# Kernel optimization log

Hardware: AMD Instinct MI355X
Metric: run time of the kernel (lower is better)

Reference implementation:

```python
import jax, jax.numpy as jnp
import numpy as np

N = 4096      # nodes
HID = 512     # hidden_size
HEADS = 8
DH = HID // HEADS
EPS = 1e-5    # BatchNorm eps


def setup_inputs() -> dict:
    key = jax.random.key(0)
    ks = jax.random.split(key, 16)
    h = jax.random.normal(ks[0], (N, HID), jnp.float32)
    # sparse adjacency (~degree 32) with self-loops so every row has a neighbor
    A = (jax.random.uniform(ks[1], (N, N)) < 0.008).astype(jnp.float32)
    A = jnp.maximum(A, jnp.eye(N, dtype=jnp.float32))
    w = lambda k, shp: jax.random.normal(k, shp, jnp.float32) * 0.02
    return {
        "A": A, "h": h,
        "Wq": w(ks[2], (HID, HID)), "bq": jnp.zeros((HID,), jnp.float32),
        "Wk": w(ks[3], (HID, HID)), "bk": jnp.zeros((HID,), jnp.float32),
        "Wv": w(ks[4], (HID, HID)), "bv": jnp.zeros((HID,), jnp.float32),
        "Wo": w(ks[5], (HID, HID)), "bo": jnp.zeros((HID,), jnp.float32),
        "bn1_g": jnp.ones((HID,), jnp.float32), "bn1_b": jnp.zeros((HID,), jnp.float32),
        "bn2_g": jnp.ones((HID,), jnp.float32), "bn2_b": jnp.zeros((HID,), jnp.float32),
        "W1": w(ks[6], (HID, 2 * HID)), "b1": jnp.zeros((2 * HID,), jnp.float32),
        "W2": w(ks[7], (2 * HID, HID)), "b2": jnp.zeros((HID,), jnp.float32),
    }


def _batchnorm(x, g, b):
    # BatchNorm1d training mode: stats over the node (batch) axis
    m = jnp.mean(x, axis=0)
    v = jnp.var(x, axis=0)
    return g * (x - m) * jax.lax.rsqrt(v + EPS) + b


def _layer(A, h, Wq, bq, Wk, bk, Wv, bv, Wo, bo,
           bn1_g, bn1_b, bn2_g, bn2_b, W1, b1, W2, b2):
    n = h.shape[0]
    q = (h @ Wq + bq).reshape(n, HEADS, DH)
    k = (h @ Wk + bk).reshape(n, HEADS, DH)
    v = (h @ Wv + bv).reshape(n, HEADS, DH)
    # scores [heads, n, m], masked by adjacency
    scores = jnp.einsum('nhd,mhd->hnm', q, k) / np.float32(np.sqrt(DH))
    scores = jnp.where(A[None, :, :] > 0, scores, jnp.float32(-1e9))
    attn = jax.nn.softmax(scores, axis=-1)
    o = jnp.einsum('hnm,mhd->nhd', attn, v).reshape(n, HID)
    h1 = o @ Wo + bo
    h = _batchnorm(h + h1, bn1_g, bn1_b)
    h2 = jax.nn.relu(h @ W1 + b1) @ W2 + b2
    return _batchnorm(h + h2, bn2_g, bn2_b)


def reference(A, h, Wq, bq, Wk, bk, Wv, bv, Wo, bo,
              bn1_g, bn1_b, bn2_g, bn2_b, W1, b1, W2, b2):
    return _layer(A, h, Wq, bq, Wk, bk, Wv, bv, Wo, bo,
                  bn1_g, bn1_b, bn2_g, bn2_b, W1, b1, W2, b2)
```

## Files before the change

### kernel.cpp

```cpp
#include <hip/hip_runtime.h>

#define N_NODES 4096
#define HID 512
#define HEADS 8
#define DH 64
#define EPS 1e-5f
#define MAXD 128

typedef __attribute__((ext_vector_type(8))) short bf16x8;
typedef __attribute__((ext_vector_type(4))) float f32x4;

__device__ __forceinline__ unsigned short f2bf(float f) {
    unsigned int u = __float_as_uint(f);
    unsigned int r = (u + 0x7FFFu + ((u >> 16) & 1u)) >> 16;
    return (unsigned short)r;
}
__device__ __forceinline__ float blo(unsigned int u) {
    return __uint_as_float(u << 16);
}
__device__ __forceinline__ float bhi(unsigned int u) {
    return __uint_as_float(u & 0xffff0000u);
}

__device__ __forceinline__ void gld_lds16(const void* g, void* l) {
    __builtin_amdgcn_global_load_lds(
        (const __attribute__((address_space(1))) unsigned int*)g,
        (__attribute__((address_space(3))) unsigned int*)l, 16, 0, 0);
}

template<int TM, int EPI>
__global__ __launch_bounds__(256) void gemm_bf16(
    const unsigned short* __restrict__ Xb, const unsigned short* __restrict__ Wt,
    const float* __restrict__ bias, const float* __restrict__ res,
    const unsigned short* __restrict__ resb,
    float* __restrict__ outf, unsigned short* __restrict__ outb,
    float* __restrict__ sum, float* __restrict__ sumsq,
    int K, int Nc)
{
    constexpr int WM = TM / 64;
    __shared__ __align__(16) unsigned short As[TM * 64];
    __shared__ __align__(16) unsigned short Bs[64 * 64];

    const int tid = threadIdx.x;
    const int lane = tid & 63;
    const int wv = tid >> 6;
    const int m0 = blockIdx.y * TM, n0 = blockIdx.x * 64;
    const int lc = lane & 15, lq = lane >> 4;
    const int rowbase = wv * (WM * 16);

    const int srow = tid >> 3;
    const int schunk = (tid & 7) ^ (srow & 7);
    unsigned short* ldsA = As + tid * 8;
    unsigned short* ldsB = Bs + tid * 8;
    const int rs0 = lq ^ (lc & 7);
    const int rs1 = (4 + lq) ^ (lc & 7);

    f32x4 acc[WM][4] = {};

    for (int k0 = 0; k0 < K; k0 += 64) {
        const unsigned short* gA = Xb + (size_t)(m0 + srow) * K + k0 + schunk * 8;
        const unsigned short* gB = Wt + (size_t)(n0 + srow) * K + k0 + schunk * 8;
        #pragma unroll
        for (int p = 0; p < TM / 32; ++p)
            gld_lds16(gA + (size_t)(p * 32) * K, ldsA + p * 2048);
        #pragma unroll
        for (int p = 0; p < 2; ++p)
            gld_lds16(gB + (size_t)(p * 32) * K, ldsB + p * 2048);
        __syncthreads();

        #pragma unroll
        for (int hh = 0; hh < 2; ++hh) {
            const int rs = hh ? rs1 : rs0;
            bf16x8 af[WM], bfr[4];
            #pragma unroll
            for (int i = 0; i < WM; ++i)
                af[i] = *(const bf16x8*)&As[(rowbase + i * 16 + lc) * 64 + rs * 8];
            #pragma unroll
            for (int j = 0; j < 4; ++j)
                bfr[j] = *(const bf16x8*)&Bs[(j * 16 + lc) * 64 + rs * 8];
            #pragma unroll
            for (int i = 0; i < WM; ++i)
                #pragma unroll
                for (int j = 0; j < 4; ++j)
                    acc[i][j] = __builtin_amdgcn_mfma_f32_16x16x32_bf16(af[i], bfr[j], acc[i][j], 0, 0, 0);
        }
        __syncthreads();
    }

    float cs[4] = {}, css[4] = {};
    #pragma unroll
    for (int i = 0; i < WM; ++i) {
        #pragma unroll
        for (int j = 0; j < 4; ++j) {
            const int gr0 = m0 + rowbase + i * 16 + lq * 4;
            const int gc = n0 + j * 16 + lc;
            const float bi = bias[gc];
            #pragma unroll
            for (int r = 0; r < 4; ++r) {
                float val = acc[i][j][r] + bi;
                size_t off = (size_t)(gr0 + r) * Nc + gc;
                if (EPI == 0)      outb[off] = f2bf(val);
                else if (EPI == 1) outb[off] = f2bf(fmaxf(val, 0.f));
                else {
                    if (EPI == 2) val += res[off];
                    else          val += blo((unsigned int)resb[off]);
                    outf[off] = val;
                    cs[j] += val; css[j] += val * val;
                }
            }
        }
    }
    if (EPI >= 2) {
        #pragma unroll
        for (int j = 0; j < 4; ++j) {
            float s = cs[j], ss = css[j];
            s += __shfl_xor(s, 16); s += __shfl_xor(s, 32);
            ss += __shfl_xor(ss, 16); ss += __shfl_xor(ss, 32);
            if (lq == 0) {
                const int gc = n0 + j * 16 + lc;
                atomicAdd(&sum[gc], s);
                atomicAdd(&sumsq[gc], ss);
            }
        }
    }
}

__global__ __launch_bounds__(256) void prep_all(
    const float* __restrict__ Wq, const float* __restrict__ Wk,
    const float* __restrict__ Wv, const float* __restrict__ Wo,
    const float* __restrict__ W1, const float* __restrict__ W2,
    const float* __restrict__ h,
    const float* __restrict__ bq, const float* __restrict__ bk,
    const float* __restrict__ bv,
    unsigned short* __restrict__ wqkvT, unsigned short* __restrict__ woT,
    unsigned short* __restrict__ w1T, unsigned short* __restrict__ w2T,
    unsigned int* __restrict__ hb, float* __restrict__ bqkv,
    float* __restrict__ st)
{
    const int z = blockIdx.z;
    if (z < 6) {
        const float* in; unsigned short* out; int R, C;
        switch (z) {
            case 0: in = Wq; out = wqkvT;          R = 512;  C = 512;  break;
            case 1: in = Wk; out = wqkvT + 262144; R = 512;  C = 512;  break;
            case 2: in = Wv; out = wqkvT + 524288; R = 512;  C = 512;  break;
            case 3: in = Wo; out = woT;            R = 512;  C = 512;  break;
            case 4: in = W1; out = w1T;            R = 512;  C = 1024; break;
            default: in = W2; out = w2T;           R = 1024; C = 512;  break;
        }
        const int bc = blockIdx.x * 32, br = blockIdx.y * 32;
        if (bc >= C || br >= R) return;
        __shared__ float tile[32][33];
        const int tx = threadIdx.x & 31, ty = threadIdx.x >> 5;
        #pragma unroll
        for (int r = ty; r < 32; r += 8)
            tile[r][tx] = in[(size_t)(br + r) * C + bc + tx];
        __syncthreads();
        #pragma unroll
        for (int r = ty; r < 32; r += 8)
            out[(size_t)(bc + r) * R + br + tx] = f2bf(tile[tx][r]);
    } else if (z == 6) {
        const int blk = blockIdx.y * 32 + blockIdx.x;
        const int i = blk * 512 + threadIdx.x * 2;
        const float4* in4 = (const float4*)h;
        #pragma unroll
        for (int u = 0; u < 2; ++u) {
            float4 f = in4[i + u];
            hb[(i + u) * 2]     = (unsigned int)f2bf(f.x) | ((unsigned int)f2bf(f.y) << 16);
            hb[(i + u) * 2 + 1] = (unsigned int)f2bf(f.z) | ((unsigned int)f2bf(f.w) << 16);
        }
    } else {
        const int blk = blockIdx.y * 32 + blockIdx.x;
        const int i = blk * 256 + threadIdx.x;
        if (i < 1536) bqkv[i] = i < 512 ? bq[i] : (i < 1024 ? bk[i - 512] : bv[i - 1024]);
        if (i < 2048) st[i] = 0.0f;
    }
}

__global__ __launch_bounds__(256) void sparse_attn5(
    const float* __restrict__ A, const unsigned short* __restrict__ qkv,
    unsigned short* __restrict__ o)
{
    const int n = blockIdx.x;
    const int tid = threadIdx.x;
    const int wv = tid >> 6, lane = tid & 63;

    __shared__ int s_idx[MAXD];
    __shared__ float s_p[8][MAXD];
    __shared__ int s_cnt[4];

    const float4* r4 = (const float4*)(A + (size_t)n * N_NODES);
    float4 av[4];
    #pragma unroll
    for (int t = 0; t < 4; ++t)
        av[t] = r4[wv * 256 + t * 64 + lane];

    const unsigned long long lt = (1ull << lane) - 1ull;
    int cnt = 0;
    #pragma unroll
    for (int t = 0; t < 4; ++t) {
        #pragma unroll
        for (int b = 0; b < 4; ++b) {
            float vb = (b == 0) ? av[t].x : (b == 1) ? av[t].y : (b == 2) ? av[t].z : av[t].w;
            cnt += __popcll(__ballot(vb > 0.0f));
        }
    }
    if (lane == 0) s_cnt[wv] = cnt;
    __syncthreads();
    int base = 0, total = 0;
    #pragma unroll
    for (int w = 0; w < 4; ++w) {
        if (w < wv) base += s_cnt[w];
        total += s_cnt[w];
    }
    const int d = total < MAXD ? total : MAXD;
    #pragma unroll
    for (int t = 0; t < 4; ++t) {
        #pragma unroll
        for (int b = 0; b < 4; ++b) {
            float vb = (b == 0) ? av[t].x : (b == 1) ? av[t].y : (b == 2) ? av[t].z : av[t].w;
            unsigned long long m = __ballot(vb > 0.0f);
            if (vb > 0.0f) {
                int p = base + __popcll(m & lt);
                if (p < MAXD) s_idx[p] = wv * 1024 + t * 256 + lane * 4 + b;
            }
            base += __popcll(m);
        }
    }
    __syncthreads();

    const int jl = lane >> 3;
    const int dgs = lane & 7;
    const int jl2 = lane >> 4;
    const int dga = lane & 15;
    const int h0 = wv, h1 = wv + 4;

    const unsigned short* qp = qkv + (size_t)n * 1536 + dgs * 8;
    uint4 qa = *(const uint4*)(qp + h0 * 64);
    uint4 qb = *(const uint4*)(qp + h1 * 64);
    const float a0 = blo(qa.x), a1 = bhi(qa.x), a2 = blo(qa.y), a3 = bhi(qa.y);
    const float a4 = blo(qa.z), a5 = bhi(qa.z), a6 = blo(qa.w), a7 = bhi(qa.w);
    const float b0 = blo(qb.x), b1 = bhi(qb.x), b2 = blo(qb.y), b3 = bhi(qb.y);
    const float b4 = blo(qb.z), b5 = bhi(qb.z), b6 = blo(qb.w), b7 = bhi(qb.w);

    uint4 ka = {0, 0, 0, 0}, kb = {0, 0, 0, 0};
    if (jl < d) {
        const unsigned short* p = qkv + (size_t)s_idx[jl] * 1536 + 512 + dgs * 8;
        ka = *(const uint4*)(p + h0 * 64);
        kb = *(const uint4*)(p + h1 * 64);
    }
    for (int j0 = 0; j0 < d; j0 += 8) {
        const uint4 ca = ka, cb = kb;
        const int jn = j0 + 8 + jl;
        if (jn < d) {
            const unsigned short* p = qkv + (size_t)s_idx[jn] * 1536 + 512 + dgs * 8;
            ka = *(const uint4*)(p + h0 * 64);
            kb = *(const uint4*)(p + h1 * 64);
        }
        const int jc = j0 + jl;
        float s0 = 0.f, s1 = 0.f;
        if (jc < d) {
            s0 = a0 * blo(ca.x) + a1 * bhi(ca.x) + a2 * blo(ca.y) + a3 * bhi(ca.y)
               + a4 * blo(ca.z) + a5 * bhi(ca.z) + a6 * blo(ca.w) + a7 * bhi(ca.w);
            s1 = b0 * blo(cb.x) + b1 * bhi(cb.x) + b2 * blo(cb.y) + b3 * bhi(cb.y)
               + b4 * blo(cb.z) + b5 * bhi(cb.z) + b6 * blo(cb.w) + b7 * bhi(cb.w);
        }
        s0 += __shfl_xor(s0, 1); s1 += __shfl_xor(s1, 1);
        s0 += __shfl_xor(s0, 2); s1 += __shfl_xor(s1, 2);
        s0 += __shfl_xor(s0, 4); s1 += __shfl_xor(s1, 4);
        if (dgs == 0 && jc < d) {
            s_p[h0][jc] = s0 * 0.125f;
            s_p[h1][jc] = s1 * 0.125f;
        }
    }

    float inv0, inv1;
    #pragma unroll
    for (int hh = 0; hh < 2; ++hh) {
        float* sp = s_p[hh ? h1 : h0];
        float mx = -1e30f;
        for (int j = lane; j < d; j += 64) mx = fmaxf(mx, sp[j]);
        #pragma unroll
        for (int off = 32; off; off >>= 1) mx = fmaxf(mx, __shfl_xor(mx, off));
        float sum = 0.f;
        for (int j = lane; j < d; j += 64) {
            float e = __expf(sp[j] - mx);
            sp[j] = e;
            sum += e;
        }
        #pragma unroll
        for (int off = 32; off; off >>= 1) sum += __shfl_xor(sum, off);
        if (hh) inv1 = 1.0f / sum; else inv0 = 1.0f / sum;
    }

    float x0 = 0.f, x1 = 0.f, x2 = 0.f, x3 = 0.f;
    float y0 = 0.f, y1 = 0.f, y2 = 0.f, y3 = 0.f;
    uint2 va = {0, 0}, vb = {0, 0};
    if (jl2 < d) {
        const unsigned short* p = qkv + (size_t)s_idx[jl2] * 1536 + 1024 + dga * 4;
        va = *(const uint2*)(p + h0 * 64);
        vb = *(const uint2*)(p + h1 * 64);
    }
    for (int j0 = 0; j0 < d; j0 += 4) {
        const uint2 ca = va, cb = vb;
        const int jn = j0 + 4 + jl2;
        if (jn < d) {
            const unsigned short* p = qkv + (size_t)s_idx[jn] * 1536 + 1024 + dga * 4;
            va = *(const uint2*)(p + h0 * 64);
            vb = *(const uint2*)(p + h1 * 64);
        }
        const int jc = j0 + jl2;
        if (jc < d) {
            const float p0 = s_p[h0][jc], p1 = s_p[h1][jc];
            x0 += p0 * blo(ca.x); x1 += p0 * bhi(ca.x);
            x2 += p0 * blo(ca.y); x3 += p0 * bhi(ca.y);
            y0 += p1 * blo(cb.x); y1 += p1 * bhi(cb.x);
            y2 += p1 * blo(cb.y); y3 += p1 * bhi(cb.y);
        }
    }
    x0 += __shfl_xor(x0, 16); x0 += __shfl_xor(x0, 32);
    x1 += __shfl_xor(x1, 16); x1 += __shfl_xor(x1, 32);
    x2 += __shfl_xor(x2, 16); x2 += __shfl_xor(x2, 32);
    x3 += __shfl_xor(x3, 16); x3 += __shfl_xor(x3, 32);
    y0 += __shfl_xor(y0, 16); y0 += __shfl_xor(y0, 32);
    y1 += __shfl_xor(y1, 16); y1 += __shfl_xor(y1, 32);
    y2 += __shfl_xor(y2, 16); y2 += __shfl_xor(y2, 32);
    y3 += __shfl_xor(y3, 16); y3 += __shfl_xor(y3, 32);
    if (jl2 == 0) {
        uint2 w0, w1;
        w0.x = (unsigned int)f2bf(x0 * inv0) | ((unsigned int)f2bf(x1 * inv0) << 16);
        w0.y = (unsigned int)f2bf(x2 * inv0) | ((unsigned int)f2bf(x3 * inv0) << 16);
        w1.x = (unsigned int)f2bf(y0 * inv1) | ((unsigned int)f2bf(y1 * inv1) << 16);
        w1.y = (unsigned int)f2bf(y2 * inv1) | ((unsigned int)f2bf(y3 * inv1) << 16);
        *(uint2*)(o + (size_t)n * 512 + h0 * 64 + dga * 4) = w0;
        *(uint2*)(o + (size_t)n * 512 + h1 * 64 + dga * 4) = w1;
    }
}

__global__ __launch_bounds__(256) void bn_apply4(
    const float4* __restrict__ x, const float* __restrict__ sum,
    const float* __restrict__ sumsq, const float* __restrict__ g,
    const float* __restrict__ b, float4* __restrict__ yf,
    uint2* __restrict__ yb)
{
    const int i = blockIdx.x * 256 + threadIdx.x;
    const int c4 = i & 127;
    const float4 s4 = ((const float4*)sum)[c4];
    const float4 q4 = ((const float4*)sumsq)[c4];
    const float4 g4 = ((const float4*)g)[c4];
    const float4 b4 = ((const float4*)b)[c4];
    const float4 xv = x[i];
    const float kN = 1.0f / N_NODES;
    float4 r;
    { float m = s4.x * kN; r.x = g4.x * (xv.x - m) * rsqrtf(q4.x * kN - m * m + EPS) + b4.x; }
    { float m = s4.y * kN; r.y = g4.y * (xv.y - m) * rsqrtf(q4.y * kN - m * m + EPS) + b4.y; }
    { float m = s4.z * kN; r.z = g4.z * (xv.z - m) * rsqrtf(q4.z * kN - m * m + EPS) + b4.z; }
    { float m = s4.w * kN; r.w = g4.w * (xv.w - m) * rsqrtf(q4.w * kN - m * m + EPS) + b4.w; }
    if (yf) yf[i] = r;
    if (yb) {
        uint2 p;
        p.x = (unsigned int)f2bf(r.x) | ((unsigned int)f2bf(r.y) << 16);
        p.y = (unsigned int)f2bf(r.z) | ((unsigned int)f2bf(r.w) << 16);
        yb[i] = p;
    }
}


extern "C" void kernel_launch(void* const* d_in, const int* in_sizes, int n_in,
                              void* d_out, int out_size, void* d_ws, size_t ws_size,
                              hipStream_t stream)
{
    const float* A   = (const float*)d_in[0];
    const float* h   = (const float*)d_in[1];
    const float* Wq  = (const float*)d_in[2];
    const float* bq  = (const float*)d_in[3];
    const float* Wk  = (const float*)d_in[4];
    const float* bk  = (const float*)d_in[5];
    const float* Wv  = (const float*)d_in[6];
    const float* bv  = (const float*)d_in[7];
    const float* Wo  = (const float*)d_in[8];
    const float* bo  = (const float*)d_in[9];
    const float* g1  = (const float*)d_in[10];
    const float* b1g = (const float*)d_in[11];
    const float* g2  = (const float*)d_in[12];
    const float* b2g = (const float*)d_in[13];
    const float* W1  = (const float*)d_in[14];
    const float* b1  = (const float*)d_in[15];
    const float* W2  = (const float*)d_in[16];
    const float* b2  = (const float*)d_in[17];
    float* out = (float*)d_out;

    float* ws = (float*)d_ws;
    unsigned short* hb    = (unsigned short*)(ws);
    unsigned short* qkvb  = (unsigned short*)(ws + 1048576);
    unsigned short* o_bf  = (unsigned short*)(ws + 4194304);
    unsigned short* wqkvT = (unsigned short*)(ws + 5242880);
    unsigned short* woT   = (unsigned short*)(ws + 5636096);
    unsigned short* w1T   = (unsigned short*)(ws + 5767168);
    unsigned short* w2T   = (unsigned short*)(ws + 6029312);
    unsigned short* t_b   = (unsigned short*)(ws + 6291456);
    float* x1   = ws + 8388608;
    float* x2   = ws + 10485760;
    unsigned short* xb1_b = (unsigned short*)(ws + 12582912);
    float* bqkv = ws + 13631488;
    float* st   = ws + 13633024;

    prep_all<<<dim3(32, 32, 8), dim3(256), 0, stream>>>(
        Wq, Wk, Wv, Wo, W1, W2, h, bq, bk, bv,
        wqkvT, woT, w1T, w2T, (unsigned int*)hb, bqkv, st);

    gemm_bf16<128, 0><<<dim3(24, 32), dim3(256), 0, stream>>>(
        hb, wqkvT, bqkv, nullptr, nullptr, nullptr, qkvb, nullptr, nullptr, 512, 1536);

    sparse_attn5<<<dim3(N_NODES), dim3(256), 0, stream>>>(A, qkvb, o_bf);

    gemm_bf16<64, 2><<<dim3(8, 64), dim3(256), 0, stream>>>(
        o_bf, woT, bo, h, nullptr, x1, nullptr, st, st + 512, 512, 512);

    bn_apply4<<<dim3(2048), dim3(256), 0, stream>>>(
        (const float4*)x1, st, st + 512, g1, b1g, nullptr, (uint2*)xb1_b);

    gemm_bf16<128, 1><<<dim3(16, 32), dim3(256), 0, stream>>>(
        xb1_b, w1T, b1, nullptr, nullptr, nullptr, t_b, nullptr, nullptr, 512, 1024);

    gemm_bf16<64, 3><<<dim3(8, 64), dim3(256), 0, stream>>>(
        t_b, w2T, b2, nullptr, xb1_b, x2, nullptr, st + 1024, st + 1536, 1024, 512);

    bn_apply4<<<dim3(2048), dim3(256), 0, stream>>>(
        (const float4*)x2, st + 1024, st + 1536, g2, b2g, (float4*)out, nullptr);

    (void)in_sizes; (void)n_in; (void)out_size; (void)ws_size;
}
```

Before: 232.9 us.

## Replace LDS-staged GEMM with single-wave direct-global-load MFMA kernel

The bf16 GEMM drops its shared-memory staging (global_load_lds plus swizzled LDS reads and two block barriers per k-step). Each 64-thread block now computes a small TMx64 tile, loading MFMA fragments straight from global memory into registers. The grids are resized to many more, smaller blocks. This removes barrier and LDS overhead and raises block count, but gives up data reuse across waves, so each operand is fetched from global or L2 more times, and the loads are strided 16-byte per-lane accesses.

```diff
diff --git a/kernel.cpp b/kernel.cpp
--- a/kernel.cpp
+++ b/kernel.cpp
@@ -22,14 +22,8 @@
     return __uint_as_float(u & 0xffff0000u);
 }
 
-__device__ __forceinline__ void gld_lds16(const void* g, void* l) {
-    __builtin_amdgcn_global_load_lds(
-        (const __attribute__((address_space(1))) unsigned int*)g,
-        (__attribute__((address_space(3))) unsigned int*)l, 16, 0, 0);
-}
-
 template<int TM, int EPI>
-__global__ __launch_bounds__(256) void gemm_bf16(
+__global__ __launch_bounds__(64) void gemm_w1(
     const unsigned short* __restrict__ Xb, const unsigned short* __restrict__ Wt,
     const float* __restrict__ bias, const float* __restrict__ res,
     const unsigned short* __restrict__ resb,
@@ -37,54 +31,36 @@
     float* __restrict__ sum, float* __restrict__ sumsq,
     int K, int Nc)
 {
-    constexpr int WM = TM / 64;
-    __shared__ __align__(16) unsigned short As[TM * 64];
-    __shared__ __align__(16) unsigned short Bs[64 * 64];
-
-    const int tid = threadIdx.x;
-    const int lane = tid & 63;
-    const int wv = tid >> 6;
+    constexpr int WM = TM / 16;
+    const int lane = threadIdx.x;
     const int m0 = blockIdx.y * TM, n0 = blockIdx.x * 64;
     const int lc = lane & 15, lq = lane >> 4;
-    const int rowbase = wv * (WM * 16);
-
-    const int srow = tid >> 3;
-    const int schunk = (tid & 7) ^ (srow & 7);
-    unsigned short* ldsA = As + tid * 8;
-    unsigned short* ldsB = Bs + tid * 8;
-    const int rs0 = lq ^ (lc & 7);
-    const int rs1 = (4 + lq) ^ (lc & 7);
+
+    const unsigned short* pa = Xb + (size_t)(m0 + lc) * K + lq * 8;
+    const unsigned short* pb = Wt + (size_t)(n0 + lc) * K + lq * 8;
 
     f32x4 acc[WM][4] = {};
 
     for (int k0 = 0; k0 < K; k0 += 64) {
-        const unsigned short* gA = Xb + (size_t)(m0 + srow) * K + k0 + schunk * 8;
-        const unsigned short* gB = Wt + (size_t)(n0 + srow) * K + k0 + schunk * 8;
-        #pragma unroll
-        for (int p = 0; p < TM / 32; ++p)
-            gld_lds16(gA + (size_t)(p * 32) * K, ldsA + p * 2048);
-        #pragma unroll
-        for (int p = 0; p < 2; ++p)
-            gld_lds16(gB + (size_t)(p * 32) * K, ldsB + p * 2048);
-        __syncthreads();
-
-        #pragma unroll
-        for (int hh = 0; hh < 2; ++hh) {
-            const int rs = hh ? rs1 : rs0;
-            bf16x8 af[WM], bfr[4];
+        bf16x8 af[WM][2], bfr[4][2];
+        #pragma unroll
+        for (int i = 0; i < WM; ++i)
             #pragma unroll
-            for (int i = 0; i < WM; ++i)
-                af[i] = *(const bf16x8*)&As[(rowbase + i * 16 + lc) * 64 + rs * 8];
+            for (int h = 0; h < 2; ++h)
+                af[i][h] = *(const bf16x8*)(pa + (size_t)(i * 16) * K + k0 + h * 32);
+        #pragma unroll
+        for (int j = 0; j < 4; ++j)
             #pragma unroll
-            for (int j = 0; j < 4; ++j)
-                bfr[j] = *(const bf16x8*)&Bs[(j * 16 + lc) * 64 + rs * 8];
+            for (int h = 0; h < 2; ++h)
+                bfr[j][h] = *(const bf16x8*)(pb + (size_t)(j * 16) * K + k0 + h * 32);
+        #pragma unroll
+        for (int h = 0; h < 2; ++h)
             #pragma unroll
             for (int i = 0; i < WM; ++i)
                 #pragma unroll
                 for (int j = 0; j < 4; ++j)
-                    acc[i][j] = __builtin_amdgcn_mfma_f32_16x16x32_bf16(af[i], bfr[j], acc[i][j], 0, 0, 0);
-        }
-        __syncthreads();
+                    acc[i][j] = __builtin_amdgcn_mfma_f32_16x16x32_bf16(
+                        af[i][h], bfr[j][h], acc[i][j], 0, 0, 0);
     }
 
     float cs[4] = {}, css[4] = {};
@@ -92,7 +68,7 @@
     for (int i = 0; i < WM; ++i) {
         #pragma unroll
         for (int j = 0; j < 4; ++j) {
-            const int gr0 = m0 + rowbase + i * 16 + lq * 4;
+            const int gr0 = m0 + i * 16 + lq * 4;
             const int gc = n0 + j * 16 + lc;
             const float bi = bias[gc];
             #pragma unroll
@@ -409,21 +385,21 @@
         Wq, Wk, Wv, Wo, W1, W2, h, bq, bk, bv,
         wqkvT, woT, w1T, w2T, (unsigned int*)hb, bqkv, st);
 
-    gemm_bf16<128, 0><<<dim3(24, 32), dim3(256), 0, stream>>>(
+    gemm_w1<64, 0><<<dim3(24, 64), dim3(64), 0, stream>>>(
         hb, wqkvT, bqkv, nullptr, nullptr, nullptr, qkvb, nullptr, nullptr, 512, 1536);
 
     sparse_attn5<<<dim3(N_NODES), dim3(256), 0, stream>>>(A, qkvb, o_bf);
 
-    gemm_bf16<64, 2><<<dim3(8, 64), dim3(256), 0, stream>>>(
+    gemm_w1<32, 2><<<dim3(8, 128), dim3(64), 0, stream>>>(
         o_bf, woT, bo, h, nullptr, x1, nullptr, st, st + 512, 512, 512);
 
     bn_apply4<<<dim3(2048), dim3(256), 0, stream>>>(
         (const float4*)x1, st, st + 512, g1, b1g, nullptr, (uint2*)xb1_b);
 
-    gemm_bf16<128, 1><<<dim3(16, 32), dim3(256), 0, stream>>>(
+    gemm_w1<32, 1><<<dim3(16, 128), dim3(64), 0, stream>>>(
         xb1_b, w1T, b1, nullptr, nullptr, nullptr, t_b, nullptr, nullptr, 512, 1024);
 
-    gemm_bf16<64, 3><<<dim3(8, 64), dim3(256), 0, stream>>>(
+    gemm_w1<32, 3><<<dim3(8, 128), dim3(64), 0, stream>>>(
         t_b, w2T, b2, nullptr, xb1_b, x2, nullptr, st + 1024, st + 1536, 1024, 512);
 
     bn_apply4<<<dim3(2048), dim3(256), 0, stream>>>(
```

After: 271.3 us. +16.5%, slower.

## Fuse first BatchNorm into FFN GEMMs and load A fragments directly from pre-tiled layout

Applied to the files above, without the earlier changes.

The first BatchNorm apply kernel is removed. Its normalization is folded into the W1 GEMM's A-operand load, which reads fp32 x1 and applies a per-channel scale/shift table before converting to bf16, and into the W2 GEMM's residual epilogue. The h and attention-output bf16 buffers are now written in an MFMA-fragment-tiled layout, so the QKV and Wo GEMMs load A straight into registers with double buffering instead of staging through LDS. This drops one kernel launch and a round trip of the intermediate through memory. In exchange, the W1 GEMM reads fp32 A with extra ALU and scattered LDS lookups, and the A loads bypass shared memory reuse.

```diff
diff --git a/kernel.cpp b/kernel.cpp
--- a/kernel.cpp
+++ b/kernel.cpp
@@ -28,71 +28,135 @@
         (__attribute__((address_space(3))) unsigned int*)l, 16, 0, 0);
 }
 
-template<int TM, int EPI>
-__global__ __launch_bounds__(256) void gemm_bf16(
-    const unsigned short* __restrict__ Xb, const unsigned short* __restrict__ Wt,
+
+template<int TM, int EPI, int AMODE, int K>
+__global__ __launch_bounds__(256) void gemm_h(
+    const unsigned short* __restrict__ Xb, const float* __restrict__ Xf,
+    const unsigned short* __restrict__ Wt,
     const float* __restrict__ bias, const float* __restrict__ res,
-    const unsigned short* __restrict__ resb,
     float* __restrict__ outf, unsigned short* __restrict__ outb,
     float* __restrict__ sum, float* __restrict__ sumsq,
-    int K, int Nc)
+    const float* __restrict__ bsum, const float* __restrict__ bsumsq,
+    const float* __restrict__ bg, const float* __restrict__ bb,
+    int Nc)
 {
     constexpr int WM = TM / 64;
-    __shared__ __align__(16) unsigned short As[TM * 64];
+    constexpr int KC = K >> 5;
+    constexpr int NS = K >> 6;
     __shared__ __align__(16) unsigned short Bs[64 * 64];
+    __shared__ float2 lut[(AMODE == 2) ? K : 4];
 
     const int tid = threadIdx.x;
     const int lane = tid & 63;
     const int wv = tid >> 6;
     const int m0 = blockIdx.y * TM, n0 = blockIdx.x * 64;
     const int lc = lane & 15, lq = lane >> 4;
-    const int rowbase = wv * (WM * 16);
+    const int wrow = m0 + wv * (TM / 4);
 
     const int srow = tid >> 3;
     const int schunk = (tid & 7) ^ (srow & 7);
-    unsigned short* ldsA = As + tid * 8;
     unsigned short* ldsB = Bs + tid * 8;
-    const int rs0 = lq ^ (lc & 7);
-    const int rs1 = (4 + lq) ^ (lc & 7);
-
+
+    const unsigned short* paf = Xb + ((size_t)(wrow >> 4) * KC) * 512 + lane * 8;
+    const unsigned short* par = Xb + (size_t)(wrow + lc) * K + lq * 8;
+    const float* parf = Xf + (size_t)(wrow + lc) * K + lq * 8;
+
+    if (AMODE == 2) {
+        #pragma unroll
+        for (int c = tid; c < K; c += 256) {
+            float m = bsum[c] * (1.0f / N_NODES);
+            float v = bsumsq[c] * (1.0f / N_NODES) - m * m;
+            float iv = rsqrtf(v + EPS);
+            float sc = bg[c] * iv;
+            lut[c] = make_float2(sc, bb[c] - sc * m);
+        }
+        __syncthreads();
+    }
+
+    bf16x8 afb[2][WM][2];
     f32x4 acc[WM][4] = {};
 
-    for (int k0 = 0; k0 < K; k0 += 64) {
-        const unsigned short* gA = Xb + (size_t)(m0 + srow) * K + k0 + schunk * 8;
-        const unsigned short* gB = Wt + (size_t)(n0 + srow) * K + k0 + schunk * 8;
-        #pragma unroll
-        for (int p = 0; p < TM / 32; ++p)
-            gld_lds16(gA + (size_t)(p * 32) * K, ldsA + p * 2048);
-        #pragma unroll
-        for (int p = 0; p < 2; ++p)
-            gld_lds16(gB + (size_t)(p * 32) * K, ldsB + p * 2048);
+#define LOAD_A(S, BUF)                                                          \
+    if (AMODE != 2) {                                                           \
+        _Pragma("unroll")                                                       \
+        for (int i = 0; i < WM; ++i)                                            \
+            _Pragma("unroll")                                                   \
+            for (int h = 0; h < 2; ++h)                                         \
+                afb[BUF][i][h] = (AMODE == 1)                                   \
+                    ? *(const bf16x8*)(paf + ((size_t)i * KC + 2 * (S) + h) * 512) \
+                    : *(const bf16x8*)(par + (size_t)(i * 16) * K + (S) * 64 + h * 32); \
+    }
+
+    LOAD_A(0, 0)
+    #pragma unroll
+    for (int s = 0; s < NS; ++s) {
+        const unsigned short* gB = Wt + (size_t)(n0 + srow) * K + s * 64 + schunk * 8;
+        gld_lds16(gB, ldsB);
+        gld_lds16(gB + (size_t)32 * K, ldsB + 2048);
         __syncthreads();
 
-        #pragma unroll
-        for (int hh = 0; hh < 2; ++hh) {
-            const int rs = hh ? rs1 : rs0;
-            bf16x8 af[WM], bfr[4];
+        if (s + 1 < NS) { LOAD_A(s + 1, ((s & 1) ^ 1)) }
+
+        bf16x8 afx[WM][2];
+        if (AMODE == 2) {
             #pragma unroll
             for (int i = 0; i < WM; ++i)
-                af[i] = *(const bf16x8*)&As[(rowbase + i * 16 + lc) * 64 + rs * 8];
+                #pragma unroll
+                for (int h = 0; h < 2; ++h) {
+                    const float* p = parf + (size_t)(i * 16) * K + s * 64 + h * 32;
+                    float4 f0 = *(const float4*)p;
+                    float4 f1 = *(const float4*)(p + 4);
+                    const int kb = s * 64 + h * 32 + lq * 8;
+                    float2 l0 = lut[kb], l1 = lut[kb + 1], l2 = lut[kb + 2], l3 = lut[kb + 3];
+                    float2 l4 = lut[kb + 4], l5 = lut[kb + 5], l6 = lut[kb + 6], l7 = lut[kb + 7];
+                    uint4 uu;
+                    uu.x = (unsigned int)f2bf(f0.x * l0.x + l0.y) | ((unsigned int)f2bf(f0.y * l1.x + l1.y) << 16);
+                    uu.y = (unsigned int)f2bf(f0.z * l2.x + l2.y) | ((unsigned int)f2bf(f0.w * l3.x + l3.y) << 16);
+                    uu.z = (unsigned int)f2bf(f1.x * l4.x + l4.y) | ((unsigned int)f2bf(f1.y * l5.x + l5.y) << 16);
+                    uu.w = (unsigned int)f2bf(f1.z * l6.x + l6.y) | ((unsigned int)f2bf(f1.w * l7.x + l7.y) << 16);
+                    afx[i][h] = *(bf16x8*)&uu;
+                }
+        }
+
+        bf16x8 bfr[4][2];
+        #pragma unroll
+        for (int j = 0; j < 4; ++j)
             #pragma unroll
-            for (int j = 0; j < 4; ++j)
-                bfr[j] = *(const bf16x8*)&Bs[(j * 16 + lc) * 64 + rs * 8];
+            for (int h = 0; h < 2; ++h)
+                bfr[j][h] = *(const bf16x8*)&Bs[(j * 16 + lc) * 64 + ((h * 4 + lq) ^ (lc & 7)) * 8];
+
+        #pragma unroll
+        for (int h = 0; h < 2; ++h)
             #pragma unroll
             for (int i = 0; i < WM; ++i)
                 #pragma unroll
                 for (int j = 0; j < 4; ++j)
-                    acc[i][j] = __builtin_amdgcn_mfma_f32_16x16x32_bf16(af[i], bfr[j], acc[i][j], 0, 0, 0);
-        }
+                    acc[i][j] = __builtin_amdgcn_mfma_f32_16x16x32_bf16(
+                        (AMODE == 2) ? afx[i][h] : afb[s & 1][i][h],
+                        bfr[j][h], acc[i][j], 0, 0, 0);
         __syncthreads();
     }
+#undef LOAD_A
+
+    float scj[4], shj[4];
+    if (EPI == 4) {
+        #pragma unroll
+        for (int j = 0; j < 4; ++j) {
+            const int gc = n0 + j * 16 + lc;
+            float m = bsum[gc] * (1.0f / N_NODES);
+            float v = bsumsq[gc] * (1.0f / N_NODES) - m * m;
+            float iv = rsqrtf(v + EPS);
+            scj[j] = bg[gc] * iv;
+            shj[j] = bb[gc] - scj[j] * m;
+        }
+    }
 
     float cs[4] = {}, css[4] = {};
     #pragma unroll
     for (int i = 0; i < WM; ++i) {
         #pragma unroll
         for (int j = 0; j < 4; ++j) {
-            const int gr0 = m0 + rowbase + i * 16 + lq * 4;
+            const int gr0 = wrow + i * 16 + lq * 4;
             const int gc = n0 + j * 16 + lc;
             const float bi = bias[gc];
             #pragma unroll
@@ -103,7 +167,7 @@
                 else if (EPI == 1) outb[off] = f2bf(fmaxf(val, 0.f));
                 else {
                     if (EPI == 2) val += res[off];
-                    else          val += blo((unsigned int)resb[off]);
+                    else          val += scj[j] * res[off] + shj[j];
                     outf[off] = val;
                     cs[j] += val; css[j] += val * val;
                 }
@@ -163,12 +227,16 @@
         const int blk = blockIdx.y * 32 + blockIdx.x;
         const int i = blk * 512 + threadIdx.x * 2;
         const float4* in4 = (const float4*)h;
-        #pragma unroll
-        for (int u = 0; u < 2; ++u) {
-            float4 f = in4[i + u];
-            hb[(i + u) * 2]     = (unsigned int)f2bf(f.x) | ((unsigned int)f2bf(f.y) << 16);
-            hb[(i + u) * 2 + 1] = (unsigned int)f2bf(f.z) | ((unsigned int)f2bf(f.w) << 16);
-        }
+        float4 f0 = in4[i], f1 = in4[i + 1];
+        uint4 w;
+        w.x = (unsigned int)f2bf(f0.x) | ((unsigned int)f2bf(f0.y) << 16);
+        w.y = (unsigned int)f2bf(f0.z) | ((unsigned int)f2bf(f0.w) << 16);
+        w.z = (unsigned int)f2bf(f1.x) | ((unsigned int)f2bf(f1.y) << 16);
+        w.w = (unsigned int)f2bf(f1.z) | ((unsigned int)f2bf(f1.w) << 16);
+        const int m = i >> 7, k = (i & 127) * 4;
+        const size_t off_u4 = ((size_t)(m >> 4) * 16 + (k >> 5)) * 64
+                            + ((k >> 3) & 3) * 16 + (m & 15);
+        ((uint4*)hb)[off_u4] = w;
     } else {
         const int blk = blockIdx.y * 32 + blockIdx.x;
         const int i = blk * 256 + threadIdx.x;
@@ -177,7 +245,7 @@
     }
 }
 
-__global__ __launch_bounds__(256) void sparse_attn5(
+__global__ __launch_bounds__(256) void sparse_attn7(
     const float* __restrict__ A, const unsigned short* __restrict__ qkv,
     unsigned short* __restrict__ o)
 {
@@ -231,8 +299,6 @@
 
     const int jl = lane >> 3;
     const int dgs = lane & 7;
-    const int jl2 = lane >> 4;
-    const int dga = lane & 15;
     const int h0 = wv, h1 = wv + 4;
 
     const unsigned short* qp = qkv + (size_t)n * 1536 + dgs * 8;
@@ -293,6 +359,8 @@
         if (hh) inv1 = 1.0f / sum; else inv0 = 1.0f / sum;
     }
 
+    const int jl2 = lane >> 4;
+    const int dga = lane & 15;
     float x0 = 0.f, x1 = 0.f, x2 = 0.f, x3 = 0.f;
     float y0 = 0.f, y1 = 0.f, y2 = 0.f, y3 = 0.f;
     uint2 va = {0, 0}, vb = {0, 0};
@@ -332,16 +400,18 @@
         w0.y = (unsigned int)f2bf(x2 * inv0) | ((unsigned int)f2bf(x3 * inv0) << 16);
         w1.x = (unsigned int)f2bf(y0 * inv1) | ((unsigned int)f2bf(y1 * inv1) << 16);
         w1.y = (unsigned int)f2bf(y2 * inv1) | ((unsigned int)f2bf(y3 * inv1) << 16);
-        *(uint2*)(o + (size_t)n * 512 + h0 * 64 + dga * 4) = w0;
-        *(uint2*)(o + (size_t)n * 512 + h1 * 64 + dga * 4) = w1;
+        const int k0 = h0 * 64 + dga * 4;
+        const int k1 = h1 * 64 + dga * 4;
+        const size_t base_n = (size_t)(n >> 4) * 16 * 512 + (n & 15) * 8;
+        *(uint2*)(o + base_n + (size_t)(k0 >> 5) * 512 + ((k0 >> 3) & 3) * 128 + (k0 & 7)) = w0;
+        *(uint2*)(o + base_n + (size_t)(k1 >> 5) * 512 + ((k1 >> 3) & 3) * 128 + (k1 & 7)) = w1;
     }
 }
 
 __global__ __launch_bounds__(256) void bn_apply4(
     const float4* __restrict__ x, const float* __restrict__ sum,
     const float* __restrict__ sumsq, const float* __restrict__ g,
-    const float* __restrict__ b, float4* __restrict__ yf,
-    uint2* __restrict__ yb)
+    const float* __restrict__ b, float4* __restrict__ yf)
 {
     const int i = blockIdx.x * 256 + threadIdx.x;
     const int c4 = i & 127;
@@ -356,13 +426,7 @@
     { float m = s4.y * kN; r.y = g4.y * (xv.y - m) * rsqrtf(q4.y * kN - m * m + EPS) + b4.y; }
     { float m = s4.z * kN; r.z = g4.z * (xv.z - m) * rsqrtf(q4.z * kN - m * m + EPS) + b4.z; }
     { float m = s4.w * kN; r.w = g4.w * (xv.w - m) * rsqrtf(q4.w * kN - m * m + EPS) + b4.w; }
-    if (yf) yf[i] = r;
-    if (yb) {
-        uint2 p;
-        p.x = (unsigned int)f2bf(r.x) | ((unsigned int)f2bf(r.y) << 16);
-        p.y = (unsigned int)f2bf(r.z) | ((unsigned int)f2bf(r.w) << 16);
-        yb[i] = p;
-    }
+    yf[i] = r;
 }
 
 
@@ -401,7 +465,6 @@
     unsigned short* t_b   = (unsigned short*)(ws + 6291456);
     float* x1   = ws + 8388608;
     float* x2   = ws + 10485760;
-    unsigned short* xb1_b = (unsigned short*)(ws + 12582912);
     float* bqkv = ws + 13631488;
     float* st   = ws + 13633024;
 
@@ -409,25 +472,26 @@
         Wq, Wk, Wv, Wo, W1, W2, h, bq, bk, bv,
         wqkvT, woT, w1T, w2T, (unsigned int*)hb, bqkv, st);
 
-    gemm_bf16<128, 0><<<dim3(24, 32), dim3(256), 0, stream>>>(
-        hb, wqkvT, bqkv, nullptr, nullptr, nullptr, qkvb, nullptr, nullptr, 512, 1536);
-
-    sparse_attn5<<<dim3(N_NODES), dim3(256), 0, stream>>>(A, qkvb, o_bf);
-
-    gemm_bf16<64, 2><<<dim3(8, 64), dim3(256), 0, stream>>>(
-        o_bf, woT, bo, h, nullptr, x1, nullptr, st, st + 512, 512, 512);
+    gemm_h<128, 0, 1, 512><<<dim3(24, 32), dim3(256), 0, stream>>>(
+        hb, nullptr, wqkvT, bqkv, nullptr, nullptr, qkvb,
+        nullptr, nullptr, nullptr, nullptr, nullptr, nullptr, 1536);
+
+    sparse_attn7<<<dim3(N_NODES), dim3(256), 0, stream>>>(A, qkvb, o_bf);
+
+    gemm_h<64, 2, 1, 512><<<dim3(8, 64), dim3(256), 0, stream>>>(
+        o_bf, nullptr, woT, bo, h, x1, nullptr,
+        st, st + 512, nullptr, nullptr, nullptr, nullptr, 512);
+
+    gemm_h<128, 1, 2, 512><<<dim3(16, 32), dim3(256), 0, stream>>>(
+        nullptr, x1, w1T, b1, nullptr, nullptr, t_b,
+        nullptr, nullptr, st, st + 512, g1, b1g, 1024);
+
+    gemm_h<64, 4, 0, 1024><<<dim3(8, 64), dim3(256), 0, stream>>>(
+        t_b, nullptr, w2T, b2, x1, x2, nullptr,
+        st + 1024, st + 1536, st, st + 512, g1, b1g, 512);
 
     bn_apply4<<<dim3(2048), dim3(256), 0, stream>>>(
-        (const float4*)x1, st, st + 512, g1, b1g, nullptr, (uint2*)xb1_b);
-
-    gemm_bf16<128, 1><<<dim3(16, 32), dim3(256), 0, stream>>>(
-        xb1_b, w1T, b1, nullptr, nullptr, nullptr, t_b, nullptr, nullptr, 512, 1024);
-
-    gemm_bf16<64, 3><<<dim3(8, 64), dim3(256), 0, stream>>>(
-        t_b, w2T, b2, nullptr, xb1_b, x2, nullptr, st + 1024, st + 1536, 1024, 512);
-
-    bn_apply4<<<dim3(2048), dim3(256), 0, stream>>>(
-        (const float4*)x2, st + 1024, st + 1536, g2, b2g, (float4*)out, nullptr);
+        (const float4*)x2, st + 1024, st + 1536, g2, b2g, (float4*)out);
 
     (void)in_sizes; (void)n_in; (void)out_size; (void)ws_size;
 }
```

Measured after the change: 240.3 us. 3.2% more time.
